# Performance work log

Hardware: AMD Instinct MI355X
Metric: run time of the kernel (lower is better)

The kernel has to match this reference:

```python
import jax, jax.numpy as jnp
import numpy as np

N, E, IN, OUT, R = 50000, 800000, 256, 256, 8
BN_EPS = 1e-5


def setup_inputs() -> dict:
    key = jax.random.key(0)
    ks = jax.random.split(key, 8)
    x = jax.random.normal(ks[0], (N, IN), dtype=jnp.float32)
    edge_index = jax.random.randint(ks[1], (2, E), 0, N, dtype=jnp.int64)
    # edge_attr: 5 float columns; column 4 carries the relation id in [0, R)
    edge_attr = jax.random.randint(ks[2], (E, 5), 0, R).astype(jnp.float32)
    # RGCNConv params (PyG defaults: root_weight=True, bias=True, aggr='mean')
    W = jax.random.normal(ks[3], (R, IN, OUT), dtype=jnp.float32) / np.sqrt(IN)
    root = jax.random.normal(ks[4], (IN, OUT), dtype=jnp.float32) / np.sqrt(IN)
    bias = jnp.zeros((OUT,), dtype=jnp.float32)
    # BatchNorm1d affine params
    gamma = jnp.ones((OUT,), dtype=jnp.float32)
    beta = jnp.zeros((OUT,), dtype=jnp.float32)
    # PReLU single shared slope (torch default init 0.25)
    prelu_a = jnp.asarray(0.25, dtype=jnp.float32)
    return {"x": x, "edge_index": edge_index, "edge_attr": edge_attr,
            "W": W, "root": root, "bias": bias,
            "gamma": gamma, "beta": beta, "prelu_a": prelu_a}


def _rgcn_block(x, edge_index, edge_type, W, root, bias, gamma, beta, prelu_a):
    src, dst = edge_index[0], edge_index[1]
    # per-(relation, dst) mean aggregation via a single segment_sum
    seg = edge_type.astype(jnp.int32) * N + dst.astype(jnp.int32)  # [E]
    msg_sum = jax.ops.segment_sum(x[src], seg, num_segments=R * N)  # [R*N, IN]
    cnt = jax.ops.segment_sum(jnp.ones((E,), x.dtype), seg, num_segments=R * N)
    mean = msg_sum.reshape(R, N, IN) / jnp.maximum(cnt, 1.0).reshape(R, N, 1)
    # relation-specific linear transforms, summed over relations, plus root + bias
    h = jnp.einsum('rni,rio->no', mean, W) + x @ root + bias  # [N, OUT]
    # BatchNorm1d (training mode: batch statistics over nodes)
    mu = jnp.mean(h, axis=0)
    var = jnp.mean(jnp.square(h - mu), axis=0)
    h = (h - mu) * jax.lax.rsqrt(var + BN_EPS) * gamma + beta
    # PReLU (single shared slope); dropout is identity at inference
    h = jnp.where(h > 0, h, prelu_a * h)
    # residual (in_channels == out_channels -> Identity projection)
    return h + x


def reference(x, edge_index, edge_attr, W, root, bias, gamma, beta, prelu_a):
    edge_type = edge_attr[:, 4].astype(jnp.int32)
    return _rgcn_block(x, edge_index, edge_type, W, root, bias, gamma, beta, prelu_a)
```

## Files before the change

kernel.cpp:

```cpp
#include <hip/hip_runtime.h>
#include <cstdio>
#include <cstdint>


constexpr int kN  = 50000;
constexpr int kE  = 800000;
constexpr int kR  = 8;
constexpr int kC  = 256;
constexpr int kMP = 50048;
constexpr int kK  = 2304;
constexpr int kWG = (kMP / 128) * (kC / 128);

typedef __attribute__((ext_vector_type(8))) short bf16x8;
typedef __attribute__((ext_vector_type(4))) float f32x4;
typedef __attribute__((ext_vector_type(2))) unsigned int u32x2;

__device__ __forceinline__ unsigned short f2bf(float f) {
  unsigned u = __builtin_bit_cast(unsigned, f);
  u = u + 0x7FFFu + ((u >> 16) & 1u);
  return (unsigned short)(u >> 16);
}
__device__ __forceinline__ float bf2f(unsigned short s) {
  unsigned u = ((unsigned)s) << 16;
  return __builtin_bit_cast(float, u);
}
__device__ __forceinline__ void gload16(const void* g, void* l) {
  __builtin_amdgcn_global_load_lds((__attribute__((address_space(1))) const void*)g,
                                   (__attribute__((address_space(3))) void*)l, 16, 0, 0);
}

__global__ void k_count(const int* __restrict__ ei, const float* __restrict__ ea,
                        int* __restrict__ cnt) {
  int e = blockIdx.x * blockDim.x + threadIdx.x;
  if (e >= kE) return;
  int dst = ei[kE + e];
  int rel = (int)ea[(size_t)e * 5 + 4];
  if ((unsigned)dst >= (unsigned)kN || (unsigned)rel >= (unsigned)kR) return;
  atomicAdd(&cnt[rel * kN + dst], 1);
}

__global__ void k_convert_x(const float* __restrict__ x, unsigned short* __restrict__ A) {
  int i = (blockIdx.x * blockDim.x + threadIdx.x) * 4;
  if (i >= kN * kC) return;
  int row = i >> 8, col = i & 255;
  float4 v = *(const float4*)(x + i);
  ushort4 o;
  o.x = f2bf(v.x); o.y = f2bf(v.y); o.z = f2bf(v.z); o.w = f2bf(v.w);
  *(ushort4*)(A + (size_t)row * kK + 2048 + col) = o;
}

__global__ void k_convert_w(const float* __restrict__ W, const float* __restrict__ root,
                            unsigned short* __restrict__ wbfT) {
  int t = blockIdx.x * blockDim.x + threadIdx.x;
  if (t >= kC * kK) return;
  int c = t / kK, k = t - c * kK;
  float v;
  if (k < kR * kC) {
    int r = k >> 8, kk = k & 255;
    v = W[(size_t)r * kC * kC + (size_t)kk * kC + c];
  } else {
    v = root[(size_t)(k - kR * kC) * kC + c];
  }
  wbfT[(size_t)c * kK + k] = f2bf(v);
}

__global__ void k_grp(const int* __restrict__ cnt, int* __restrict__ cursor,
                      int* __restrict__ off, int* __restrict__ cur) {
  int t = blockIdx.x * blockDim.x + threadIdx.x;
  int lane = threadIdx.x & 63;
  int c[kR];
  int gsz = 0;
  if (t < kN) {
#pragma unroll
    for (int r = 0; r < kR; ++r) { c[r] = cnt[r * kN + t]; gsz += c[r]; }
  } else {
#pragma unroll
    for (int r = 0; r < kR; ++r) c[r] = 0;
  }
  int incl = gsz;
#pragma unroll
  for (int d = 1; d < 64; d <<= 1) {
    int v = __shfl_up(incl, d);
    if (lane >= d) incl += v;
  }
  int wtot = __shfl(incl, 63);
  int base = 0;
  if (lane == 63) base = atomicAdd(cursor, wtot);
  base = __shfl(base, 63);
  if (t < kN) {
    int o = base + incl - gsz;
    off[t] = o;
#pragma unroll
    for (int r = 0; r < kR; ++r) { cur[r * kN + t] = o; o += c[r]; }
  }
}

__global__ void k_fill(const int* __restrict__ ei, const float* __restrict__ ea,
                       int* __restrict__ cur, unsigned short* __restrict__ ebuf) {
  int e = blockIdx.x * blockDim.x + threadIdx.x;
  if (e >= kE) return;
  int src = ei[e];
  int dst = ei[kE + e];
  int rel = (int)ea[(size_t)e * 5 + 4];
  if ((unsigned)dst >= (unsigned)kN || (unsigned)rel >= (unsigned)kR) return;
  int pos = atomicAdd(&cur[rel * kN + dst], 1);
  ebuf[pos] = (unsigned short)src;
}

__global__ __launch_bounds__(256) void k_agg(const unsigned short* __restrict__ ebuf,
                                             const int* __restrict__ off,
                                             const int* __restrict__ cnt,
                                             unsigned short* A) {
  int dst = blockIdx.x * 4 + (threadIdx.x >> 6);
  if (dst >= kN) return;
  int lane = threadIdx.x & 63;
  int e = off[dst];
  const unsigned short* xcols = A + 2048 + lane * 4;
  unsigned short* mrow = A + (size_t)dst * kK + lane * 4;
#pragma unroll
  for (int r = 0; r < kR; ++r) {
    int c = cnt[r * kN + dst];
    float s0 = 0.f, s1 = 0.f, s2 = 0.f, s3 = 0.f;
    for (int k = 0; k < c; ++k) {
      int src = ebuf[e + k];
      ushort4 v = *(const ushort4*)(xcols + (size_t)src * kK);
      s0 += bf2f(v.x); s1 += bf2f(v.y); s2 += bf2f(v.z); s3 += bf2f(v.w);
    }
    e += c;
    float sc = c > 0 ? 1.f / (float)c : 0.f;
    unsigned lo = (unsigned)f2bf(s0 * sc) | ((unsigned)f2bf(s1 * sc) << 16);
    unsigned hi = (unsigned)f2bf(s2 * sc) | ((unsigned)f2bf(s3 * sc) << 16);
    u32x2 pk = {lo, hi};
    __builtin_nontemporal_store(pk, (u32x2*)(mrow + r * 256));
  }
}

__global__ __launch_bounds__(512) void k_gemm(const unsigned short* __restrict__ A,
                                              const unsigned short* __restrict__ wbfT,
                                              float* __restrict__ out,
                                              const float* __restrict__ bias,
                                              float* __restrict__ cs,
                                              float* __restrict__ csq) {
  __shared__ __align__(16) unsigned short As[2][128 * 64];
  __shared__ __align__(16) unsigned short Bs[2][128 * 64];
  const int tid = threadIdx.x;
  const int lane = tid & 63, wv = tid >> 6;
  const int bid = blockIdx.x;
  const int xcd = bid & 7, idx = bid >> 3;
  const int wgid = (xcd < 6 ? xcd * 98 : 588 + (xcd - 6) * 97) + idx;
  const int n0 = (wgid & 1) * 128, m0 = (wgid >> 1) * 128;
  const int wm = wv >> 2, wn = wv & 3;
  f32x4 acc[4][2] = {};

  const int lrow = tid >> 3;
  const int skk  = ((tid & 7) ^ (lrow & 7)) * 8;

#define STAGE(buf, kt)                                                            \
  {                                                                               \
    const int kb_ = (kt) * 64;                                                    \
    _Pragma("unroll")                                                             \
    for (int c = 0; c < 2; ++c) {                                                 \
      int l_   = tid + 512 * c;                                      \
      int row_ = c * 64 + lrow;                                      \
      gload16(A    + (size_t)(m0 + row_) * kK + kb_ + skk, &As[buf][l_ * 8]);     \
      gload16(wbfT + (size_t)(n0 + row_) * kK + kb_ + skk, &Bs[buf][l_ * 8]);     \
    }                                                                             \
  }

  STAGE(0, 0);
  constexpr int NT = kK / 64;
  for (int t = 0; t < NT; ++t) {
    const int buf = t & 1;
    if (t + 1 < NT) {
      STAGE(buf ^ 1, t + 1);
      asm volatile("s_waitcnt vmcnt(4)" ::: "memory");
    } else {
      asm volatile("s_waitcnt vmcnt(0)" ::: "memory");
    }
    __builtin_amdgcn_s_barrier();
    __builtin_amdgcn_sched_barrier(0);
#pragma unroll
    for (int kk = 0; kk < 64; kk += 32) {
      const int koff = kk + (lane >> 4) * 8;
      bf16x8 a[4], b[2];
#pragma unroll
      for (int i = 0; i < 4; ++i) {
        int ra = wm * 64 + i * 16 + (lane & 15);
        unsigned ba = (unsigned)(koff * 2) ^ (unsigned)((ra & 7) << 4);
        a[i] = *(const bf16x8*)((const char*)As[buf] + ra * 128 + ba);
      }
#pragma unroll
      for (int j = 0; j < 2; ++j) {
        int rb = wn * 32 + j * 16 + (lane & 15);
        unsigned bb = (unsigned)(koff * 2) ^ (unsigned)((rb & 7) << 4);
        b[j] = *(const bf16x8*)((const char*)Bs[buf] + rb * 128 + bb);
      }
#pragma unroll
      for (int i = 0; i < 4; ++i)
#pragma unroll
        for (int j = 0; j < 2; ++j)
          acc[i][j] = __builtin_amdgcn_mfma_f32_16x16x32_bf16(a[i], b[j], acc[i][j], 0, 0, 0);
    }
    __builtin_amdgcn_s_barrier();
    __builtin_amdgcn_sched_barrier(0);
  }
#undef STAGE

#pragma unroll
  for (int j = 0; j < 2; ++j) {
    int col = n0 + wn * 32 + j * 16 + (lane & 15);
    float bv = bias[col];
    float s = 0.f, ss = 0.f;
#pragma unroll
    for (int i = 0; i < 4; ++i) {
      int rb = m0 + wm * 64 + i * 16 + (lane >> 4) * 4;
#pragma unroll
      for (int q = 0; q < 4; ++q) {
        float v = acc[i][j][q];
        s += v; ss += v * v;
        int row = rb + q;
        if (row < kN) out[(size_t)row * kC + col] = v + bv;
      }
    }
    s  += __shfl_xor(s, 16);  s  += __shfl_xor(s, 32);
    ss += __shfl_xor(ss, 16); ss += __shfl_xor(ss, 32);
    if (lane < 16) { atomicAdd(&cs[col], s); atomicAdd(&csq[col], ss); }
  }
}

__global__ void k_final(float* __restrict__ h, const float* __restrict__ x,
                        const float* __restrict__ cs, const float* __restrict__ csq,
                        const float* __restrict__ bias,
                        const float* __restrict__ gamma, const float* __restrict__ beta,
                        const float* __restrict__ prelu) {
  int idx = (blockIdx.x * blockDim.x + threadIdx.x) * 4;
  if (idx >= kN * kC) return;
  int col = idx & 255;
  const float inv_n = 1.0f / (float)kN;
  float a = prelu[0];
  float4 hv = *(float4*)(h + idx);
  float4 xv = *(const float4*)(x + idx);
  float hr[4] = {hv.x, hv.y, hv.z, hv.w};
  float xr[4] = {xv.x, xv.y, xv.z, xv.w};
#pragma unroll
  for (int j = 0; j < 4; ++j) {
    int c = col + j;
    float mu_raw = cs[c] * inv_n;
    float var = csq[c] * inv_n - mu_raw * mu_raw;
    float mu  = mu_raw + bias[c];
    float k   = gamma[c] * rsqrtf(var + 1e-5f);
    float v   = (hr[j] - mu) * k + beta[c];
    v = v > 0.f ? v : a * v;
    hr[j] = v + xr[j];
  }
  *(float4*)(h + idx) = make_float4(hr[0], hr[1], hr[2], hr[3]);
}

extern "C" void kernel_launch(void* const* d_in, const int* in_sizes, int n_in,
                              void* d_out, int out_size, void* d_ws, size_t ws_size,
                              hipStream_t stream) {
  const float* x     = (const float*)d_in[0];
  const int*   ei    = (const int*)d_in[1];
  const float* ea    = (const float*)d_in[2];
  const float* W     = (const float*)d_in[3];
  const float* root  = (const float*)d_in[4];
  const float* bias  = (const float*)d_in[5];
  const float* gamma = (const float*)d_in[6];
  const float* beta  = (const float*)d_in[7];
  const float* prelu = (const float*)d_in[8];
  float* out = (float*)d_out;
  char* ws = (char*)d_ws;

  size_t o = 0;
  auto alloc = [&](size_t sz) { size_t r = o; o += (sz + 255) & ~(size_t)255; return r; };
  size_t a_o    = alloc((size_t)kMP * kK * 2);
  size_t wbf_o  = alloc((size_t)kC * kK * 2);
  size_t cnt_o  = alloc((size_t)kR * kN * 4);
  size_t cs_o   = alloc(256 * 4);
  size_t csq_o  = alloc(256 * 4);
  size_t csr_o  = alloc(256);
  size_t zend   = o;
  size_t off_o  = alloc((size_t)kN * 4);
  size_t cur_o  = alloc((size_t)kR * kN * 4);
  size_t eb_o   = alloc((size_t)kE * 2);
  if (o > ws_size) {
    fprintf(stderr, "[RGCN kernel] ws too small: need %zu have %zu\n", o, ws_size);
    return;
  }

  unsigned short* A    = (unsigned short*)(ws + a_o);
  unsigned short* wbfT = (unsigned short*)(ws + wbf_o);
  int*   cnt    = (int*)(ws + cnt_o);
  float* cs     = (float*)(ws + cs_o);
  float* csq    = (float*)(ws + csq_o);
  int*   cursor = (int*)(ws + csr_o);
  int*   offp   = (int*)(ws + off_o);
  int*   cur    = (int*)(ws + cur_o);
  unsigned short* ebuf = (unsigned short*)(ws + eb_o);

  hipMemsetAsync(ws + cnt_o, 0, zend - cnt_o, stream);
  hipMemsetAsync(ws + a_o + (size_t)kN * kK * 2, 0,
                 (size_t)(kMP - kN) * kK * 2, stream);
  k_count<<<(kE + 255) / 256, 256, 0, stream>>>(ei, ea, cnt);
  k_convert_x<<<(kN * kC / 4) / 256, 256, 0, stream>>>(x, A);
  k_convert_w<<<(kC * kK + 255) / 256, 256, 0, stream>>>(W, root, wbfT);
  k_grp<<<(kN + 255) / 256, 256, 0, stream>>>(cnt, cursor, offp, cur);
  k_fill<<<(kE + 255) / 256, 256, 0, stream>>>(ei, ea, cur, ebuf);
  k_agg<<<(kN + 3) / 4, 256, 0, stream>>>(ebuf, offp, cnt, A);
  k_gemm<<<kWG, 512, 0, stream>>>(A, wbfT, out, bias, cs, csq);
  k_final<<<(kN * kC / 4) / 256, 256, 0, stream>>>(out, x, cs, csq, bias, gamma, beta, prelu);
}
```

Measured before the change: 361.6 us.

## Split aggregation per relation-destination wave and use single-buffered 256-thread GEMM

The aggregation kernel now assigns one wavefront to each (relation, destination) pair instead of looping over all relations per destination. This requires storing a per-relation start offset array, and it exposes eight times more independent waves to hide gather latency. The GEMM drops from 512 to 256 threads with 4x4 MFMA tiles per wave and removes the LDS double buffering. That halves shared memory and may raise occupancy, but global loads are no longer overlapped with compute.

```diff
diff --git a/kernel.cpp b/kernel.cpp
--- a/kernel.cpp
+++ b/kernel.cpp
@@ -65,7 +65,7 @@
 }
 
 __global__ void k_grp(const int* __restrict__ cnt, int* __restrict__ cursor,
-                      int* __restrict__ off, int* __restrict__ cur) {
+                      int* __restrict__ gst, int* __restrict__ cur) {
   int t = blockIdx.x * blockDim.x + threadIdx.x;
   int lane = threadIdx.x & 63;
   int c[kR];
@@ -89,9 +89,8 @@
   base = __shfl(base, 63);
   if (t < kN) {
     int o = base + incl - gsz;
-    off[t] = o;
-#pragma unroll
-    for (int r = 0; r < kR; ++r) { cur[r * kN + t] = o; o += c[r]; }
+#pragma unroll
+    for (int r = 0; r < kR; ++r) { gst[r * kN + t] = o; cur[r * kN + t] = o; o += c[r]; }
   }
 }
 
@@ -108,107 +107,84 @@
 }
 
 __global__ __launch_bounds__(256) void k_agg(const unsigned short* __restrict__ ebuf,
-                                             const int* __restrict__ off,
+                                             const int* __restrict__ gst,
                                              const int* __restrict__ cnt,
                                              unsigned short* A) {
-  int dst = blockIdx.x * 4 + (threadIdx.x >> 6);
-  if (dst >= kN) return;
+  int w = blockIdx.x * 4 + (threadIdx.x >> 6);
   int lane = threadIdx.x & 63;
-  int e = off[dst];
+  int r = w / kN, dst = w - r * kN;
+  int st = gst[w], c = cnt[w];
   const unsigned short* xcols = A + 2048 + lane * 4;
-  unsigned short* mrow = A + (size_t)dst * kK + lane * 4;
-#pragma unroll
-  for (int r = 0; r < kR; ++r) {
-    int c = cnt[r * kN + dst];
-    float s0 = 0.f, s1 = 0.f, s2 = 0.f, s3 = 0.f;
-    for (int k = 0; k < c; ++k) {
-      int src = ebuf[e + k];
-      ushort4 v = *(const ushort4*)(xcols + (size_t)src * kK);
-      s0 += bf2f(v.x); s1 += bf2f(v.y); s2 += bf2f(v.z); s3 += bf2f(v.w);
-    }
-    e += c;
-    float sc = c > 0 ? 1.f / (float)c : 0.f;
-    unsigned lo = (unsigned)f2bf(s0 * sc) | ((unsigned)f2bf(s1 * sc) << 16);
-    unsigned hi = (unsigned)f2bf(s2 * sc) | ((unsigned)f2bf(s3 * sc) << 16);
-    u32x2 pk = {lo, hi};
-    __builtin_nontemporal_store(pk, (u32x2*)(mrow + r * 256));
-  }
-}
-
-__global__ __launch_bounds__(512) void k_gemm(const unsigned short* __restrict__ A,
+  float s0 = 0.f, s1 = 0.f, s2 = 0.f, s3 = 0.f;
+  for (int k = 0; k < c; ++k) {
+    int src = ebuf[st + k];
+    ushort4 v = *(const ushort4*)(xcols + (size_t)src * kK);
+    s0 += bf2f(v.x); s1 += bf2f(v.y); s2 += bf2f(v.z); s3 += bf2f(v.w);
+  }
+  float sc = c > 0 ? 1.f / (float)c : 0.f;
+  unsigned lo = (unsigned)f2bf(s0 * sc) | ((unsigned)f2bf(s1 * sc) << 16);
+  unsigned hi = (unsigned)f2bf(s2 * sc) | ((unsigned)f2bf(s3 * sc) << 16);
+  u32x2 pk = {lo, hi};
+  __builtin_nontemporal_store(pk, (u32x2*)(A + (size_t)dst * kK + r * 256 + lane * 4));
+}
+
+__global__ __launch_bounds__(256) void k_gemm(const unsigned short* __restrict__ A,
                                               const unsigned short* __restrict__ wbfT,
                                               float* __restrict__ out,
                                               const float* __restrict__ bias,
                                               float* __restrict__ cs,
                                               float* __restrict__ csq) {
-  __shared__ __align__(16) unsigned short As[2][128 * 64];
-  __shared__ __align__(16) unsigned short Bs[2][128 * 64];
+  __shared__ __align__(16) unsigned short As[128 * 64];
+  __shared__ __align__(16) unsigned short Bs[128 * 64];
   const int tid = threadIdx.x;
   const int lane = tid & 63, wv = tid >> 6;
   const int bid = blockIdx.x;
   const int xcd = bid & 7, idx = bid >> 3;
   const int wgid = (xcd < 6 ? xcd * 98 : 588 + (xcd - 6) * 97) + idx;
   const int n0 = (wgid & 1) * 128, m0 = (wgid >> 1) * 128;
-  const int wm = wv >> 2, wn = wv & 3;
-  f32x4 acc[4][2] = {};
-
-  const int lrow = tid >> 3;
-  const int skk  = ((tid & 7) ^ (lrow & 7)) * 8;
-
-#define STAGE(buf, kt)                                                            \
-  {                                                                               \
-    const int kb_ = (kt) * 64;                                                    \
-    _Pragma("unroll")                                                             \
-    for (int c = 0; c < 2; ++c) {                                                 \
-      int l_   = tid + 512 * c;                                      \
-      int row_ = c * 64 + lrow;                                      \
-      gload16(A    + (size_t)(m0 + row_) * kK + kb_ + skk, &As[buf][l_ * 8]);     \
-      gload16(wbfT + (size_t)(n0 + row_) * kK + kb_ + skk, &Bs[buf][l_ * 8]);     \
-    }                                                                             \
-  }
-
-  STAGE(0, 0);
+  const int wm = wv >> 1, wn = wv & 1;
+  f32x4 acc[4][4] = {};
+
   constexpr int NT = kK / 64;
   for (int t = 0; t < NT; ++t) {
-    const int buf = t & 1;
-    if (t + 1 < NT) {
-      STAGE(buf ^ 1, t + 1);
-      asm volatile("s_waitcnt vmcnt(4)" ::: "memory");
-    } else {
-      asm volatile("s_waitcnt vmcnt(0)" ::: "memory");
+    const int kb = t * 64;
+#pragma unroll
+    for (int i = 0; i < 4; ++i) {
+      int l = tid + 256 * i;
+      int row = l >> 3;
+      int sk = ((l & 7) ^ (row & 7)) * 8;
+      gload16(A    + (size_t)(m0 + row) * kK + kb + sk, &As[l * 8]);
+      gload16(wbfT + (size_t)(n0 + row) * kK + kb + sk, &Bs[l * 8]);
     }
+    asm volatile("s_waitcnt vmcnt(0)" ::: "memory");
     __builtin_amdgcn_s_barrier();
     __builtin_amdgcn_sched_barrier(0);
 #pragma unroll
     for (int kk = 0; kk < 64; kk += 32) {
       const int koff = kk + (lane >> 4) * 8;
-      bf16x8 a[4], b[2];
+      bf16x8 a[4], b[4];
 #pragma unroll
       for (int i = 0; i < 4; ++i) {
         int ra = wm * 64 + i * 16 + (lane & 15);
         unsigned ba = (unsigned)(koff * 2) ^ (unsigned)((ra & 7) << 4);
-        a[i] = *(const bf16x8*)((const char*)As[buf] + ra * 128 + ba);
+        a[i] = *(const bf16x8*)((const char*)As + ra * 128 + ba);
+        int rb = wn * 64 + i * 16 + (lane & 15);
+        unsigned bb = (unsigned)(koff * 2) ^ (unsigned)((rb & 7) << 4);
+        b[i] = *(const bf16x8*)((const char*)Bs + rb * 128 + bb);
       }
 #pragma unroll
-      for (int j = 0; j < 2; ++j) {
-        int rb = wn * 32 + j * 16 + (lane & 15);
-        unsigned bb = (unsigned)(koff * 2) ^ (unsigned)((rb & 7) << 4);
-        b[j] = *(const bf16x8*)((const char*)Bs[buf] + rb * 128 + bb);
-      }
-#pragma unroll
       for (int i = 0; i < 4; ++i)
 #pragma unroll
-        for (int j = 0; j < 2; ++j)
+        for (int j = 0; j < 4; ++j)
           acc[i][j] = __builtin_amdgcn_mfma_f32_16x16x32_bf16(a[i], b[j], acc[i][j], 0, 0, 0);
     }
     __builtin_amdgcn_s_barrier();
     __builtin_amdgcn_sched_barrier(0);
   }
-#undef STAGE
-
-#pragma unroll
-  for (int j = 0; j < 2; ++j) {
-    int col = n0 + wn * 32 + j * 16 + (lane & 15);
+
+#pragma unroll
+  for (int j = 0; j < 4; ++j) {
+    int col = n0 + wn * 64 + j * 16 + (lane & 15);
     float bv = bias[col];
     float s = 0.f, ss = 0.f;
 #pragma unroll
@@ -280,7 +256,7 @@
   size_t csq_o  = alloc(256 * 4);
   size_t csr_o  = alloc(256);
   size_t zend   = o;
-  size_t off_o  = alloc((size_t)kN * 4);
+  size_t gst_o  = alloc((size_t)kR * kN * 4);
   size_t cur_o  = alloc((size_t)kR * kN * 4);
   size_t eb_o   = alloc((size_t)kE * 2);
   if (o > ws_size) {
@@ -294,7 +270,7 @@
   float* cs     = (float*)(ws + cs_o);
   float* csq    = (float*)(ws + csq_o);
   int*   cursor = (int*)(ws + csr_o);
-  int*   offp   = (int*)(ws + off_o);
+  int*   gst    = (int*)(ws + gst_o);
   int*   cur    = (int*)(ws + cur_o);
   unsigned short* ebuf = (unsigned short*)(ws + eb_o);
 
@@ -304,9 +280,9 @@
   k_count<<<(kE + 255) / 256, 256, 0, stream>>>(ei, ea, cnt);
   k_convert_x<<<(kN * kC / 4) / 256, 256, 0, stream>>>(x, A);
   k_convert_w<<<(kC * kK + 255) / 256, 256, 0, stream>>>(W, root, wbfT);
-  k_grp<<<(kN + 255) / 256, 256, 0, stream>>>(cnt, cursor, offp, cur);
+  k_grp<<<(kN + 255) / 256, 256, 0, stream>>>(cnt, cursor, gst, cur);
   k_fill<<<(kE + 255) / 256, 256, 0, stream>>>(ei, ea, cur, ebuf);
-  k_agg<<<(kN + 3) / 4, 256, 0, stream>>>(ebuf, offp, cnt, A);
-  k_gemm<<<kWG, 512, 0, stream>>>(A, wbfT, out, bias, cs, csq);
+  k_agg<<<(kN * kR) / 4, 256, 0, stream>>>(ebuf, gst, cnt, A);
+  k_gemm<<<kWG, 256, 0, stream>>>(A, wbfT, out, bias, cs, csq);
   k_final<<<(kN * kC / 4) / 256, 256, 0, stream>>>(out, x, cs, csq, bias, gamma, beta, prelu);
 }
```

New measurement: 403.1 us. +11.5%, slower.
